# Optimization experiments

Hardware: AMD Instinct MI355X
Metric: run time of the kernel (lower is better)

Reference implementation:

```python
import jax, jax.numpy as jnp
import numpy as np

B, CIN, N, K = 4, 64, 8192, 32
COUT, H = 64, 8
D = COUT // H  # per-head depth = 8


def setup_inputs() -> dict:
    key = jax.random.key(0)
    k1, k2, k3, k4, k5 = jax.random.split(key, 5)
    s = 1.0 / np.sqrt(CIN)
    return {
        "pcd": jax.random.normal(k1, (B, CIN, N), jnp.float32),
        "neighbors": jax.random.normal(k2, (B, CIN, N, K), jnp.float32),
        "q_w": jax.random.normal(k3, (COUT, CIN), jnp.float32) * s,
        "k_w": jax.random.normal(k4, (COUT, CIN), jnp.float32) * s,
        "v_w": jax.random.normal(k5, (COUT, CIN), jnp.float32) * s,
    }


def reference(pcd, neighbors, q_w, k_w, v_w):
    # 1x1 conv projections == channel GEMMs. Channel o splits as (h = o // D, d = o % D),
    # matching torch split_heads' view(B, H, D, N, ...).
    q = jnp.einsum('oc,bcn->bon', q_w, pcd)                      # (B, C, N)
    q = q.reshape(B, H, D, N).transpose(0, 1, 3, 2)              # (B, H, N, D)
    k = jnp.einsum('oc,bcnk->bonk', k_w, neighbors)              # (B, C, N, K)
    k = k.reshape(B, H, D, N, K).transpose(0, 1, 3, 4, 2)        # (B, H, N, K, D)
    v = jnp.einsum('oc,bcnk->bonk', v_w, neighbors)
    v = v.reshape(B, H, D, N, K).transpose(0, 1, 3, 4, 2)        # (B, H, N, K, D)

    # local_scalar_dot: per-point scores over the K neighbors, scaled softmax, aggregate.
    energy = jnp.einsum('bhnd,bhnkd->bhnk', q, k) / jnp.sqrt(jnp.float32(D))
    attn = jax.nn.softmax(energy, axis=-1)                       # (B, H, N, K)
    x = jnp.einsum('bhnk,bhnkd->bhnd', attn, v)                  # (B, H, N, D)

    # torch: reshape(B, N, H*D) after moving N forward, then permute to (B, C, N)
    x = x.transpose(0, 2, 1, 3).reshape(B, N, H * D)
    return x.transpose(0, 2, 1)                                  # (B, C_out, N)
```

## Files before the change

kernel.cpp:

```cpp
#include <hip/hip_runtime.h>

namespace {

constexpr int kN = 8192;
constexpr float kScale = 0.35355339059327373f;

typedef __attribute__((ext_vector_type(8))) short short8;
typedef __attribute__((ext_vector_type(4))) float f32x4;
using uint = unsigned int;

__device__ __forceinline__ uint bf16rn(float f) {
  const uint u = __float_as_uint(f);
  return (u + 0x7fffu + ((u >> 16) & 1u)) >> 16;
}
__device__ __forceinline__ uint pack2(float lo, float hi) {
  return bf16rn(lo) | (bf16rn(hi) << 16);
}
__device__ __forceinline__ float sx(float v, int m) {
  return __shfl_xor(v, m, 64);
}

__global__ __launch_bounds__(256, 4) void ca_mfma2(
    const float* __restrict__ pcd, const float* __restrict__ nbr,
    const float* __restrict__ q_w, const float* __restrict__ k_w,
    const float* __restrict__ v_w, float* __restrict__ out) {
  __shared__ alignas(16) ushort w_lds[2][64][64];
  __shared__ alignas(16) float q_lds[16 * 68];
  __shared__ alignas(16) float x_lds[4][68];

  const int t = threadIdx.x, wave = t >> 6, lane = t & 63;
  const int l15 = lane & 15, g = lane >> 4;
  const int chunk = blockIdx.x;
  const int b = chunk >> 9;
  const int n0 = (chunk & 511) * 16;

#pragma unroll
  for (int it = 0; it < 4; ++it) {
    const int task = it * 256 + t;
    const int W = task >> 9, m = (task >> 3) & 63, c0 = (task & 7) * 8;
    const float* src = (W ? v_w : k_w) + m * 64 + c0;
    const float4 a = *(const float4*)src;
    const float4 c = *(const float4*)(src + 4);
    const uint4 pk = make_uint4(pack2(a.x, a.y), pack2(a.z, a.w),
                                pack2(c.x, c.y), pack2(c.z, c.w));
    *(uint4*)((char*)&w_lds[W][m][0] + ((c0 * 2) ^ ((m & 7) << 4))) = pk;
  }

  if (wave == 0) {
    short8 bp[2];
#pragma unroll
    for (int ks = 0; ks < 2; ++ks) {
      float pv[8];
#pragma unroll
      for (int j = 0; j < 8; ++j)
        pv[j] = pcd[((size_t)b * 64 + ks * 32 + g * 8 + j) * kN + n0 + l15];
      const uint4 u = make_uint4(pack2(pv[0], pv[1]), pack2(pv[2], pv[3]),
                                 pack2(pv[4], pv[5]), pack2(pv[6], pv[7]));
      bp[ks] = *(const short8*)&u;
    }
    f32x4 cq[4] = {};
#pragma unroll
    for (int ks = 0; ks < 2; ++ks) {
#pragma unroll
      for (int mt = 0; mt < 4; ++mt) {
        const float* qs = q_w + (mt * 16 + l15) * 64 + ks * 32 + g * 8;
        const float4 qa = *(const float4*)qs;
        const float4 qb = *(const float4*)(qs + 4);
        const uint4 u = make_uint4(pack2(qa.x * kScale, qa.y * kScale),
                                   pack2(qa.z * kScale, qa.w * kScale),
                                   pack2(qb.x * kScale, qb.y * kScale),
                                   pack2(qb.z * kScale, qb.w * kScale));
        const short8 aq = *(const short8*)&u;
        cq[mt] =
            __builtin_amdgcn_mfma_f32_16x16x32_bf16(aq, bp[ks], cq[mt], 0, 0, 0);
      }
    }
#pragma unroll
    for (int mt = 0; mt < 4; ++mt)
      *(f32x4*)&q_lds[l15 * 68 + mt * 16 + g * 4] = cq[mt];
  }
  __syncthreads();

  for (int i = 0; i < 4; ++i) {
    const int pl = i * 4 + wave;
    const int n = n0 + pl;

    float bl[2][2][8];
    const size_t pb = (size_t)b * 16777216 + (size_t)n * 32;
#pragma unroll
    for (int ks = 0; ks < 2; ++ks)
#pragma unroll
      for (int nt = 0; nt < 2; ++nt)
#pragma unroll
        for (int j = 0; j < 8; ++j)
          bl[ks][nt][j] =
              nbr[pb + (size_t)(ks * 32 + g * 8 + j) * 262144 + nt * 16 + l15];

    f32x4 qv[4];
#pragma unroll
    for (int mt = 0; mt < 4; ++mt)
      qv[mt] = *(const f32x4*)&q_lds[pl * 68 + mt * 16 + g * 4];

    short8 bf[2][2];
#pragma unroll
    for (int ks = 0; ks < 2; ++ks)
#pragma unroll
      for (int nt = 0; nt < 2; ++nt) {
        const uint4 u = make_uint4(pack2(bl[ks][nt][0], bl[ks][nt][1]),
                                   pack2(bl[ks][nt][2], bl[ks][nt][3]),
                                   pack2(bl[ks][nt][4], bl[ks][nt][5]),
                                   pack2(bl[ks][nt][6], bl[ks][nt][7]));
        bf[ks][nt] = *(const short8*)&u;
      }

    f32x4 accK[2][4] = {};
    f32x4 accV[2][4] = {};
#pragma unroll
    for (int ks = 0; ks < 2; ++ks) {
      const int cb = ks * 64 + g * 16;
#pragma unroll
      for (int W = 0; W < 2; ++W) {
#pragma unroll
        for (int mt = 0; mt < 4; ++mt) {
          const int m = mt * 16 + l15;
          const short8 af = *(const short8*)((const char*)&w_lds[W][m][0] +
                                             (cb ^ ((m & 7) << 4)));
#pragma unroll
          for (int nt = 0; nt < 2; ++nt) {
            f32x4& acc = W ? accV[nt][mt] : accK[nt][mt];
            acc = __builtin_amdgcn_mfma_f32_16x16x32_bf16(af, bf[ks][nt], acc,
                                                          0, 0, 0);
          }
        }
      }
    }

    float p_[4][2], ps[4];
#pragma unroll
    for (int mt = 0; mt < 4; ++mt) {
#pragma unroll
      for (int nt = 0; nt < 2; ++nt) {
        float part = qv[mt].x * accK[nt][mt][0] + qv[mt].y * accK[nt][mt][1] +
                     qv[mt].z * accK[nt][mt][2] + qv[mt].w * accK[nt][mt][3];
        p_[mt][nt] = __expf(part + sx(part, 16));
      }
      ps[mt] = p_[mt][0] + p_[mt][1];
    }

    const bool b8 = (l15 & 8) != 0, b4 = (l15 & 4) != 0;
    float s0 = (b8 ? ps[2] : ps[0]) + sx(b8 ? ps[0] : ps[2], 8);
    float s1 = (b8 ? ps[3] : ps[1]) + sx(b8 ? ps[1] : ps[3], 8);
    float sm = (b4 ? s1 : s0) + sx(b4 ? s0 : s1, 4);
    sm += sx(sm, 2);
    sm += sx(sm, 1);

    float xv[16];
#pragma unroll
    for (int mt = 0; mt < 4; ++mt)
#pragma unroll
      for (int r = 0; r < 4; ++r)
        xv[mt * 4 + r] =
            p_[mt][0] * accV[0][mt][r] + p_[mt][1] * accV[1][mt][r];
    float a8[8];
#pragma unroll
    for (int j = 0; j < 8; ++j)
      a8[j] = (b8 ? xv[j + 8] : xv[j]) + sx(b8 ? xv[j] : xv[j + 8], 8);
    float a4[4];
#pragma unroll
    for (int j = 0; j < 4; ++j)
      a4[j] = (b4 ? a8[j + 4] : a8[j]) + sx(b4 ? a8[j] : a8[j + 4], 4);
    const bool b2 = (l15 & 2) != 0, b1 = (l15 & 1) != 0;
    float a2[2];
#pragma unroll
    for (int j = 0; j < 2; ++j)
      a2[j] = (b2 ? a4[j + 2] : a4[j]) + sx(b2 ? a4[j] : a4[j + 2], 2);
    const float x1 = (b1 ? a2[1] : a2[0]) + sx(b1 ? a2[0] : a2[1], 1);

    x_lds[wave][(l15 >> 2) * 16 + g * 4 + (l15 & 3)] =
        x1 * __builtin_amdgcn_rcpf(sm);
    __syncthreads();
    {
      const int o = t >> 2, jj = t & 3;
      out[((size_t)b * 64 + o) * kN + n0 + i * 4 + jj] = x_lds[jj][o];
    }
    __syncthreads();
  }
}

}

extern "C" void kernel_launch(void* const* d_in, const int* in_sizes, int n_in,
                              void* d_out, int out_size, void* d_ws,
                              size_t ws_size, hipStream_t stream) {
  const float* pcd = (const float*)d_in[0];
  const float* nbr = (const float*)d_in[1];
  const float* q_w = (const float*)d_in[2];
  const float* k_w = (const float*)d_in[3];
  const float* v_w = (const float*)d_in[4];
  float* out = (float*)d_out;

  const dim3 grid(2048);
  const dim3 block(256);
  hipLaunchKernelGGL(ca_mfma2, grid, block, 0, stream, pcd, nbr, q_w, k_w, v_w,
                     out);
}
```

Baseline: 58.89 us.

## Prefetch neighbor loads across iterations and batch output stores at block end

Neighbor loads for the next point are issued before the current point's MFMA work, giving a register double-buffer that hides global-memory latency. Each wave now handles four consecutive points. All 16 results are kept in a larger LDS buffer, which replaces the two barriers per iteration with a single barrier and one float4 store per thread. The change also raises wave priority around the MFMA block and switches bf16 conversion to the library intrinsic. The cost is higher register pressure from the prefetch buffer, which may hurt occupancy under the 4-block launch bound.

```diff
diff --git a/kernel.cpp b/kernel.cpp
--- a/kernel.cpp
+++ b/kernel.cpp
@@ -1,4 +1,5 @@
 #include <hip/hip_runtime.h>
+#include <hip/hip_bf16.h>
 
 namespace {
 
@@ -9,30 +10,45 @@
 typedef __attribute__((ext_vector_type(4))) float f32x4;
 using uint = unsigned int;
 
-__device__ __forceinline__ uint bf16rn(float f) {
-  const uint u = __float_as_uint(f);
-  return (u + 0x7fffu + ((u >> 16) & 1u)) >> 16;
-}
 __device__ __forceinline__ uint pack2(float lo, float hi) {
-  return bf16rn(lo) | (bf16rn(hi) << 16);
+  const unsigned short a =
+      __builtin_bit_cast(unsigned short, __float2bfloat16(lo));
+  const unsigned short b =
+      __builtin_bit_cast(unsigned short, __float2bfloat16(hi));
+  return (uint)a | ((uint)b << 16);
 }
 __device__ __forceinline__ float sx(float v, int m) {
   return __shfl_xor(v, m, 64);
 }
 
-__global__ __launch_bounds__(256, 4) void ca_mfma2(
+__global__ __launch_bounds__(256, 4) void ca_mfma3(
     const float* __restrict__ pcd, const float* __restrict__ nbr,
     const float* __restrict__ q_w, const float* __restrict__ k_w,
     const float* __restrict__ v_w, float* __restrict__ out) {
   __shared__ alignas(16) ushort w_lds[2][64][64];
   __shared__ alignas(16) float q_lds[16 * 68];
-  __shared__ alignas(16) float x_lds[4][68];
+  __shared__ alignas(16) float x_lds[16][68];
 
   const int t = threadIdx.x, wave = t >> 6, lane = t & 63;
   const int l15 = lane & 15, g = lane >> 4;
   const int chunk = blockIdx.x;
   const int b = chunk >> 9;
   const int n0 = (chunk & 511) * 16;
+
+  float bl[2][2][8];
+  const size_t nb_base = (size_t)b * 16777216;
+  auto issue = [&](int i) {
+    const size_t pb = nb_base + (size_t)(n0 + wave * 4 + i) * 32;
+#pragma unroll
+    for (int ks = 0; ks < 2; ++ks)
+#pragma unroll
+      for (int nt = 0; nt < 2; ++nt)
+#pragma unroll
+        for (int j = 0; j < 8; ++j)
+          bl[ks][nt][j] =
+              nbr[pb + (size_t)(ks * 32 + g * 8 + j) * 262144 + nt * 16 + l15];
+  };
+  issue(0);
 
 #pragma unroll
   for (int it = 0; it < 4; ++it) {
@@ -81,25 +97,9 @@
   }
   __syncthreads();
 
+#pragma unroll
   for (int i = 0; i < 4; ++i) {
-    const int pl = i * 4 + wave;
-    const int n = n0 + pl;
-
-    float bl[2][2][8];
-    const size_t pb = (size_t)b * 16777216 + (size_t)n * 32;
-#pragma unroll
-    for (int ks = 0; ks < 2; ++ks)
-#pragma unroll
-      for (int nt = 0; nt < 2; ++nt)
-#pragma unroll
-        for (int j = 0; j < 8; ++j)
-          bl[ks][nt][j] =
-              nbr[pb + (size_t)(ks * 32 + g * 8 + j) * 262144 + nt * 16 + l15];
-
-    f32x4 qv[4];
-#pragma unroll
-    for (int mt = 0; mt < 4; ++mt)
-      qv[mt] = *(const f32x4*)&q_lds[pl * 68 + mt * 16 + g * 4];
+    const int pl = wave * 4 + i;
 
     short8 bf[2][2];
 #pragma unroll
@@ -112,19 +112,21 @@
                                    pack2(bl[ks][nt][6], bl[ks][nt][7]));
         bf[ks][nt] = *(const short8*)&u;
       }
+    if (i < 3) issue(i + 1);
 
     f32x4 accK[2][4] = {};
     f32x4 accV[2][4] = {};
+    __builtin_amdgcn_s_setprio(1);
 #pragma unroll
     for (int ks = 0; ks < 2; ++ks) {
       const int cb = ks * 64 + g * 16;
-#pragma unroll
-      for (int W = 0; W < 2; ++W) {
+      const int swz = (l15 & 7) << 4;
+#pragma unroll
+      for (int W = 0; W < 2; ++W)
 #pragma unroll
         for (int mt = 0; mt < 4; ++mt) {
-          const int m = mt * 16 + l15;
-          const short8 af = *(const short8*)((const char*)&w_lds[W][m][0] +
-                                             (cb ^ ((m & 7) << 4)));
+          const short8 af = *(const short8*)(
+              (const char*)&w_lds[W][mt * 16 + l15][0] + (cb ^ swz));
 #pragma unroll
           for (int nt = 0; nt < 2; ++nt) {
             f32x4& acc = W ? accV[nt][mt] : accK[nt][mt];
@@ -132,16 +134,17 @@
                                                           0, 0, 0);
           }
         }
-      }
-    }
+    }
+    __builtin_amdgcn_s_setprio(0);
 
     float p_[4][2], ps[4];
 #pragma unroll
     for (int mt = 0; mt < 4; ++mt) {
+      const f32x4 qv = *(const f32x4*)&q_lds[pl * 68 + mt * 16 + g * 4];
 #pragma unroll
       for (int nt = 0; nt < 2; ++nt) {
-        float part = qv[mt].x * accK[nt][mt][0] + qv[mt].y * accK[nt][mt][1] +
-                     qv[mt].z * accK[nt][mt][2] + qv[mt].w * accK[nt][mt][3];
+        float part = qv.x * accK[nt][mt][0] + qv.y * accK[nt][mt][1] +
+                     qv.z * accK[nt][mt][2] + qv.w * accK[nt][mt][3];
         p_[mt][nt] = __expf(part + sx(part, 16));
       }
       ps[mt] = p_[mt][0] + p_[mt][1];
@@ -176,14 +179,20 @@
       a2[j] = (b2 ? a4[j + 2] : a4[j]) + sx(b2 ? a4[j] : a4[j + 2], 2);
     const float x1 = (b1 ? a2[1] : a2[0]) + sx(b1 ? a2[0] : a2[1], 1);
 
-    x_lds[wave][(l15 >> 2) * 16 + g * 4 + (l15 & 3)] =
+    x_lds[pl][(l15 >> 2) * 16 + g * 4 + (l15 & 3)] =
         x1 * __builtin_amdgcn_rcpf(sm);
-    __syncthreads();
-    {
-      const int o = t >> 2, jj = t & 3;
-      out[((size_t)b * 64 + o) * kN + n0 + i * 4 + jj] = x_lds[jj][o];
-    }
-    __syncthreads();
+  }
+
+  __syncthreads();
+
+  {
+    const int o = t >> 2, seg = t & 3;
+    float4 r;
+    r.x = x_lds[seg * 4 + 0][o];
+    r.y = x_lds[seg * 4 + 1][o];
+    r.z = x_lds[seg * 4 + 2][o];
+    r.w = x_lds[seg * 4 + 3][o];
+    *(float4*)&out[((size_t)b * 64 + o) * kN + n0 + seg * 4] = r;
   }
 }
 
@@ -201,6 +210,6 @@
 
   const dim3 grid(2048);
   const dim3 block(256);
-  hipLaunchKernelGGL(ca_mfma2, grid, block, 0, stream, pcd, nbr, q_w, k_w, v_w,
+  hipLaunchKernelGGL(ca_mfma3, grid, block, 0, stream, pcd, nbr, q_w, k_w, v_w,
                      out);
 }
```

Measured after the change: 164.6 us. 2.8x slower.
